# Kernel optimization log

Hardware: AMD Instinct MI355X
Metric: run time of the kernel (lower is better)

## Reference

```python
import jax, jax.numpy as jnp
import numpy as np
from functools import partial

B, S, D, H, DK, DV, DFF = 4, 2048, 1024, 8, 128, 128, 4096
EPS = 1e-6

def rms_norm(x):
    return x * jax.lax.rsqrt(jnp.mean(x * x, axis=-1, keepdims=True) + EPS)

def l2norm(x):
    return x * jax.lax.rsqrt(jnp.sum(x * x, axis=-1, keepdims=True) + EPS)

def setup_inputs() -> dict:
    key = jax.random.key(0)
    ks = jax.random.split(key, 16)
    w = lambda k, shp: jax.random.normal(k, shp, dtype=jnp.float32) * 0.02
    return {
        'x': jax.random.normal(ks[0], (B, S, D), dtype=jnp.float32),
        'Wq': w(ks[1], (D, H * DK)),
        'Wk': w(ks[2], (D, H * DK)),
        'Wv': w(ks[3], (D, H * DV)),
        'Wb': w(ks[4], (D, H)),
        'Wa': w(ks[5], (D, H)),
        'A_log': jnp.log(jnp.linspace(1.0, 8.0, H).astype(jnp.float32)),
        'dt_bias': jax.random.normal(ks[6], (H,), dtype=jnp.float32) * 0.1,
        'Wg': w(ks[7], (D, H * DV)),
        'o_norm_w': jnp.ones((DV,), dtype=jnp.float32),
        'Wo': w(ks[8], (H * DV, D)),
        'W_fc': w(ks[9], (D, DFF)),
        'W_proj': w(ks[10], (DFF, D)),
    }

def gated_delta_net(h, Wq, Wk, Wv, Wb, Wa, A_log, dt_bias, Wg, o_norm_w, Wo):
    b, s, _ = h.shape
    q = l2norm(jax.nn.silu(h @ Wq).reshape(b, s, H, DK))
    k = l2norm(jax.nn.silu(h @ Wk).reshape(b, s, H, DK))
    v = jax.nn.silu(h @ Wv).reshape(b, s, H, DV)
    beta = jax.nn.sigmoid(h @ Wb)                                  # [b,s,H]
    g = -jnp.exp(A_log) * jax.nn.softplus(h @ Wa + dt_bias)       # [b,s,H]
    alpha = jnp.exp(g)
    scale = DK ** -0.5

    # time-major for scan
    tm = lambda a: jnp.moveaxis(a, 1, 0)
    qs, ks_, vs, als, bts = tm(q), tm(k), tm(v), tm(alpha), tm(beta)

    def step(Sst, inp):
        q_t, k_t, v_t, a_t, b_t = inp               # [b,H,dk],[b,H,dk],[b,H,dv],[b,H],[b,H]
        Sst = Sst * a_t[..., None, None]            # decay state [b,H,dk,dv]
        kv = jnp.einsum('bhd,bhde->bhe', k_t, Sst)  # current memory readout
        delta = (v_t - kv) * b_t[..., None]
        Sst = Sst + jnp.einsum('bhd,bhe->bhde', k_t, delta)
        o_t = jnp.einsum('bhd,bhde->bhe', q_t, Sst) * scale
        return Sst, o_t

    S0 = jnp.zeros((b, H, DK, DV), dtype=h.dtype)
    _, o = jax.lax.scan(step, S0, (qs, ks_, vs, als, bts))
    o = jnp.moveaxis(o, 0, 1)                       # [b,s,H,dv]

    gate = (h @ Wg).reshape(b, s, H, DV)
    o = rms_norm(o) * o_norm_w * jax.nn.silu(gate)  # gated RMSNorm
    return o.reshape(b, s, H * DV) @ Wo

def reference(x, Wq, Wk, Wv, Wb, Wa, A_log, dt_bias, Wg, o_norm_w, Wo, W_fc, W_proj):
    ln_scale = 1.0  # config.layer_norm_scaling = False
    h = gated_delta_net(ln_scale * rms_norm(x), Wq, Wk, Wv, Wb, Wa, A_log, dt_bias, Wg, o_norm_w, Wo)
    x = x + h
    m = ln_scale * rms_norm(x)
    y = jnp.square(jax.nn.relu(m @ W_fc)) @ W_proj  # nanoGPT ReLU^2 MLP
    return x + y
```

## Files before the change

### kernel.cpp

```cpp
#include <hip/hip_runtime.h>
#include <math.h>
#include <stdint.h>

#define ROWS 8192
#define DIM  1024
#define NH   8
#define DFF_ 4096
#define EPSF 1e-6f
#define SCALEQ 0.08838834764831845f

typedef __attribute__((ext_vector_type(8))) short short8;
typedef __attribute__((ext_vector_type(4))) float f32x4;

__device__ __forceinline__ float siluf(float x) {
    float e = __expf(-x);
    return x * __builtin_amdgcn_rcpf(1.0f + e);
}
__device__ __forceinline__ unsigned short f2bf(float f) {
    uint32_t u = __float_as_uint(f);
    uint32_t r = (u + 0x7FFFu + ((u >> 16) & 1u)) >> 16;
    return (unsigned short)r;
}
__device__ __forceinline__ float bf2f(unsigned short u) {
    return __uint_as_float(((uint32_t)u) << 16);
}

__device__ __forceinline__ void async16(const void* g, void* l) {
    __builtin_amdgcn_global_load_lds(
        (const __attribute__((address_space(1))) uint32_t*)g,
        (__attribute__((address_space(3))) uint32_t*)l, 16, 0, 0);
}

__global__ void rmsnorm_bf16_kernel(const float* __restrict__ x, unsigned short* __restrict__ y) {
    int row = blockIdx.x;
    int tid = threadIdx.x;
    const float4* x4 = (const float4*)(x + (size_t)row * DIM);
    float4 v = x4[tid];
    float ss = v.x * v.x + v.y * v.y + v.z * v.z + v.w * v.w;
#pragma unroll
    for (int m = 1; m < 64; m <<= 1) ss += __shfl_xor(ss, m, 64);
    __shared__ float wss[4];
    if ((tid & 63) == 0) wss[tid >> 6] = ss;
    __syncthreads();
    float tot = wss[0] + wss[1] + wss[2] + wss[3];
    float r = rsqrtf(tot * (1.0f / 1024.0f) + EPSF);
    ushort4 o;
    o.x = f2bf(v.x * r); o.y = f2bf(v.y * r); o.z = f2bf(v.z * r); o.w = f2bf(v.w * r);
    ((ushort4*)(y + (size_t)row * DIM))[tid] = o;
}

__global__ void transpose_bf16_kernel(const float* __restrict__ W, unsigned short* __restrict__ WT,
                                      int K, int N) {
    __shared__ float tile[32][33];
    int n0 = blockIdx.x * 32, k0 = blockIdx.y * 32;
    int tx = threadIdx.x & 31, ty = threadIdx.x >> 5;
#pragma unroll
    for (int r = 0; r < 32; r += 8)
        tile[ty + r][tx] = W[(size_t)(k0 + ty + r) * N + n0 + tx];
    __syncthreads();
#pragma unroll
    for (int r = 0; r < 32; r += 8)
        WT[(size_t)(n0 + ty + r) * K + k0 + tx] = f2bf(tile[tx][ty + r]);
}

__global__ void transpose5_kernel(const float* __restrict__ s0, const float* __restrict__ s1,
                                  const float* __restrict__ s2, const float* __restrict__ s3,
                                  const float* __restrict__ s4, unsigned short* __restrict__ dst) {
    __shared__ float tile[32][33];
    int z = blockIdx.z;
    const float* W = (z == 0) ? s0 : (z == 1) ? s1 : (z == 2) ? s2 : (z == 3) ? s3 : s4;
    unsigned short* WT = dst + (size_t)z * (1u << 20);
    int n0 = blockIdx.x * 32, k0 = blockIdx.y * 32;
    int tx = threadIdx.x & 31, ty = threadIdx.x >> 5;
#pragma unroll
    for (int r = 0; r < 32; r += 8)
        tile[ty + r][tx] = W[(size_t)(k0 + ty + r) * 1024 + n0 + tx];
    __syncthreads();
#pragma unroll
    for (int r = 0; r < 32; r += 8)
        WT[(size_t)(n0 + ty + r) * 1024 + k0 + tx] = f2bf(tile[tx][ty + r]);
}

#define G256_DECL \
    __shared__ __align__(16) unsigned short AL[2][2][256 * 32]; \
    __shared__ __align__(16) unsigned short BL[2][2][256 * 32]; \
    int tid = threadIdx.x; \
    int w = tid >> 6, lane = tid & 63; \
    int wm = w >> 2, wn = w & 3; \
    int lr = lane & 15; \
    int nwgx = gridDim.x; \
    int nwg = nwgx * gridDim.y; \
    int id = blockIdx.y * nwgx + blockIdx.x; \
    int cpx = nwg >> 3; \
    int nid = (id & 7) * cpx + (id >> 3); \
    int bxs = nid % nwgx, bys = nid / nwgx; \
    int bm = bys * 256, bn = bxs * 256; \
    int stg_r = w * 32 + (lane >> 2); \
    int stg_c = ((lane & 3) ^ ((lane >> 3) & 3)) * 8; \
    const unsigned short* Ag = A + (size_t)(bm + stg_r) * K + stg_c; \
    const unsigned short* Bg = BT + (size_t)(bn + stg_r) * K + stg_c; \
    int pc = ((lane >> 4) ^ ((lr >> 1) & 3)) * 8; \
    f32x4 acc[8][4] = {}; \
    short8 bf[4], af[4]; \
    int nt = K / 64;

#define G256_STAGE_A(buf, s, kto) do { \
    async16(Ag + (kto) + (s) * 32, &AL[buf][s][(w * 2 + 0) * 512]); \
    async16(Ag + (size_t)16 * K + (kto) + (s) * 32, &AL[buf][s][(w * 2 + 1) * 512]); \
} while (0)
#define G256_STAGE_B(buf, s, kto) do { \
    async16(Bg + (kto) + (s) * 32, &BL[buf][s][(w * 2 + 0) * 512]); \
    async16(Bg + (size_t)16 * K + (kto) + (s) * 32, &BL[buf][s][(w * 2 + 1) * 512]); \
} while (0)

#define G256_READ_B(cur, s) do { \
    _Pragma("unroll") \
    for (int j = 0; j < 4; ++j) \
        bf[j] = *(const short8*)&BL[cur][s][(wn * 64 + j * 16 + lr) * 32 + pc]; \
} while (0)
#define G256_READ_A(cur, s, rh) do { \
    _Pragma("unroll") \
    for (int i = 0; i < 4; ++i) \
        af[i] = *(const short8*)&AL[cur][s][(wm * 128 + (rh) * 64 + i * 16 + lr) * 32 + pc]; \
} while (0)

#define G256_MFMA(rh) do { \
    __builtin_amdgcn_s_barrier(); \
    asm volatile("s_waitcnt lgkmcnt(0)" ::: "memory"); \
    __builtin_amdgcn_s_setprio(1); \
    _Pragma("unroll") \
    for (int i = 0; i < 4; ++i) \
        _Pragma("unroll") \
        for (int j = 0; j < 4; ++j) \
            acc[(rh) * 4 + i][j] = __builtin_amdgcn_mfma_f32_16x16x32_bf16(af[i], bf[j], acc[(rh) * 4 + i][j], 0, 0, 0); \
    __builtin_amdgcn_s_setprio(0); \
} while (0)

#define G256_MAINLOOP \
    G256_STAGE_A(0, 0, 0); G256_STAGE_B(0, 0, 0); \
    G256_STAGE_A(0, 1, 0); G256_STAGE_B(0, 1, 0); \
    asm volatile("s_waitcnt vmcnt(0)" ::: "memory"); \
    __builtin_amdgcn_s_barrier(); \
    for (int t = 0; t < nt; ++t) { \
        int cur = t & 1, nxt = cur ^ 1; \
        bool pf = (t + 1 < nt); \
        int ktn = (t + 1) * 64; \
        G256_READ_B(cur, 0); \
        G256_READ_A(cur, 0, 0); \
        if (pf) G256_STAGE_A(nxt, 0, ktn); \
        G256_MFMA(0); \
        __builtin_amdgcn_s_barrier(); \
        G256_READ_A(cur, 0, 1); \
        if (pf) G256_STAGE_B(nxt, 0, ktn); \
        G256_MFMA(1); \
        asm volatile("s_waitcnt vmcnt(4)" ::: "memory"); \
        __builtin_amdgcn_s_barrier(); \
        G256_READ_B(cur, 1); \
        G256_READ_A(cur, 1, 0); \
        if (pf) G256_STAGE_A(nxt, 1, ktn); \
        G256_MFMA(0); \
        __builtin_amdgcn_s_barrier(); \
        G256_READ_A(cur, 1, 1); \
        if (pf) G256_STAGE_B(nxt, 1, ktn); \
        G256_MFMA(1); \
        asm volatile("s_waitcnt vmcnt(4)" ::: "memory"); \
        __builtin_amdgcn_s_barrier(); \
    }

template <int EPI, typename CT>
__global__ __launch_bounds__(512, 2) void gemm256(
    const unsigned short* __restrict__ A, const unsigned short* __restrict__ BT,
    CT* __restrict__ C, const float* __restrict__ res, int M, int N, int K) {
    G256_DECL
    G256_MAINLOOP

#pragma unroll
    for (int rf = 0; rf < 8; ++rf) {
        int gr0 = bm + wm * 128 + rf * 16 + (lane >> 4) * 4;
#pragma unroll
        for (int cf = 0; cf < 4; ++cf) {
            int gc = bn + wn * 64 + cf * 16 + lr;
#pragma unroll
            for (int r = 0; r < 4; ++r) {
                float v = acc[rf][cf][r];
                size_t idx = (size_t)(gr0 + r) * N + gc;
                if (EPI == 2) v += res[idx];
                else if (EPI == 3) { float t = fmaxf(v, 0.0f); v = t * t; }
                if constexpr (sizeof(CT) == 2) C[idx] = (CT)f2bf(v);
                else C[idx] = v;
            }
        }
    }
}

__global__ __launch_bounds__(512, 2) void qkvg256(
    const unsigned short* __restrict__ A, const unsigned short* __restrict__ BT,
    unsigned short* __restrict__ oq, unsigned short* __restrict__ ok,
    unsigned short* __restrict__ ov, unsigned short* __restrict__ og, int M, int K) {
    __shared__ float sums[256 * 4];
    G256_DECL
    G256_MAINLOOP

    int bsel = bn >> 10;
    int bnl = bn & 1023;
    if (bsel < 3) {
#pragma unroll
        for (int rf = 0; rf < 8; ++rf)
#pragma unroll
            for (int cf = 0; cf < 4; ++cf)
#pragma unroll
                for (int r = 0; r < 4; ++r)
                    acc[rf][cf][r] = siluf(acc[rf][cf][r]);
    }
    bool donorm = (bsel < 2);
    if (donorm) {
#pragma unroll
        for (int rf = 0; rf < 8; ++rf) {
#pragma unroll
            for (int r = 0; r < 4; ++r) {
                float p = acc[rf][0][r] * acc[rf][0][r] + acc[rf][1][r] * acc[rf][1][r] +
                          acc[rf][2][r] * acc[rf][2][r] + acc[rf][3][r] * acc[rf][3][r];
                p += __shfl_xor(p, 1, 16);
                p += __shfl_xor(p, 2, 16);
                p += __shfl_xor(p, 4, 16);
                p += __shfl_xor(p, 8, 16);
                if (lr == 0)
                    sums[(wm * 128 + rf * 16 + (lane >> 4) * 4 + r) * 4 + wn] = p;
            }
        }
        __syncthreads();
    }
    unsigned short* C = (bsel == 0) ? oq : (bsel == 1) ? ok : (bsel == 2) ? ov : og;
#pragma unroll
    for (int rf = 0; rf < 8; ++rf) {
#pragma unroll
        for (int r = 0; r < 4; ++r) {
            int lrow = wm * 128 + rf * 16 + (lane >> 4) * 4 + r;
            float rn = 1.0f;
            if (donorm)
                rn = rsqrtf(sums[lrow * 4 + (wn & 2)] + sums[lrow * 4 + (wn & 2) + 1] + EPSF);
            size_t gr = (size_t)(bm + lrow) * 1024;
#pragma unroll
            for (int cf = 0; cf < 4; ++cf) {
                int gc = bnl + wn * 64 + cf * 16 + lr;
                C[gr + gc] = f2bf(acc[rf][cf][r] * rn);
            }
        }
    }
}

template <int EPI>
__global__ __launch_bounds__(512) void gemm128n(
    const unsigned short* __restrict__ A, const unsigned short* __restrict__ BT,
    float* __restrict__ C, const float* __restrict__ res, int M, int N, int K) {
    __shared__ __align__(16) unsigned short AL[2][128 * 64];
    __shared__ __align__(16) unsigned short BL[2][256 * 64];
    int tid = threadIdx.x;
    int w = tid >> 6, lane = tid & 63;
    int wm = w >> 2, wn = w & 3;
    int lr = lane & 15;
    int nwgx = gridDim.x;
    int nwg = nwgx * gridDim.y;
    int id = blockIdx.y * nwgx + blockIdx.x;
    int cpx = nwg >> 3;
    int nid = (id & 7) * cpx + (id >> 3);
    int bxs = nid % nwgx, bys = nid / nwgx;
    int bm = bys * 128, bn = bxs * 256;

    int arow = tid >> 3;
    int ac = ((tid & 7) ^ (arow & 7)) * 8;
    const unsigned short* Aga = A + (size_t)(bm + arow) * K + ac;
    const unsigned short* Bga = BT + (size_t)(bn + arow) * K + ac;

    int pc0 = ((0 * 4 + (lane >> 4)) ^ (lr & 7)) * 8;
    int pc1 = ((1 * 4 + (lane >> 4)) ^ (lr & 7)) * 8;

    f32x4 acc[4][4] = {};
    short8 af0[4], af1[4], bf0[4], bf1[4];
    int nt = K / 64;

#define G128_STAGE(buf, kto) do { \
    async16(Aga + (kto), &AL[buf][tid * 8]); \
    async16(Aga + (size_t)64 * K + (kto), &AL[buf][(512 + tid) * 8]); \
    async16(Bga + (kto), &BL[buf][tid * 8]); \
    async16(Bga + (size_t)64 * K + (kto), &BL[buf][(512 + tid) * 8]); \
    async16(Bga + (size_t)128 * K + (kto), &BL[buf][(1024 + tid) * 8]); \
    async16(Bga + (size_t)192 * K + (kto), &BL[buf][(1536 + tid) * 8]); \
} while (0)

    G128_STAGE(0, 0);
    asm volatile("s_waitcnt vmcnt(0)" ::: "memory");
    __builtin_amdgcn_s_barrier();
    for (int t = 0; t < nt; ++t) {
        int cur = t & 1, nxt = cur ^ 1;
        if (t + 1 < nt) G128_STAGE(nxt, (t + 1) * 64);
#pragma unroll
        for (int i = 0; i < 4; ++i) {
            af0[i] = *(const short8*)&AL[cur][(wm * 64 + i * 16 + lr) * 64 + pc0];
            af1[i] = *(const short8*)&AL[cur][(wm * 64 + i * 16 + lr) * 64 + pc1];
        }
#pragma unroll
        for (int j = 0; j < 4; ++j) {
            bf0[j] = *(const short8*)&BL[cur][(wn * 64 + j * 16 + lr) * 64 + pc0];
            bf1[j] = *(const short8*)&BL[cur][(wn * 64 + j * 16 + lr) * 64 + pc1];
        }
        asm volatile("s_waitcnt lgkmcnt(0)" ::: "memory");
        __builtin_amdgcn_sched_barrier(0);
        __builtin_amdgcn_s_setprio(1);
#pragma unroll
        for (int i = 0; i < 4; ++i)
#pragma unroll
            for (int j = 0; j < 4; ++j)
                acc[i][j] = __builtin_amdgcn_mfma_f32_16x16x32_bf16(af0[i], bf0[j], acc[i][j], 0, 0, 0);
#pragma unroll
        for (int i = 0; i < 4; ++i)
#pragma unroll
            for (int j = 0; j < 4; ++j)
                acc[i][j] = __builtin_amdgcn_mfma_f32_16x16x32_bf16(af1[i], bf1[j], acc[i][j], 0, 0, 0);
        __builtin_amdgcn_s_setprio(0);
        asm volatile("s_waitcnt vmcnt(0)" ::: "memory");
        __builtin_amdgcn_s_barrier();
    }
#undef G128_STAGE

#pragma unroll
    for (int i = 0; i < 4; ++i) {
        int gr0 = bm + wm * 64 + i * 16 + (lane >> 4) * 4;
#pragma unroll
        for (int j = 0; j < 4; ++j) {
            int gc = bn + wn * 64 + j * 16 + lr;
#pragma unroll
            for (int r = 0; r < 4; ++r) {
                float v = acc[i][j][r];
                size_t idx = (size_t)(gr0 + r) * N + gc;
                if (EPI == 2) v += res[idx];
                C[idx] = v;
            }
        }
    }
}

__global__ void gating_kernel(const float* __restrict__ o, const unsigned short* __restrict__ gate,
                              const float* __restrict__ w, unsigned short* __restrict__ ob) {
    int row = blockIdx.x;
    int tid = threadIdx.x;
    const float4* op = (const float4*)(o + (size_t)row * DIM);
    float4 v = op[tid];
    float ss = v.x * v.x + v.y * v.y + v.z * v.z + v.w * v.w;
#pragma unroll
    for (int m = 1; m < 32; m <<= 1) ss += __shfl_xor(ss, m, 32);
    float r = rsqrtf(ss * (1.0f / 128.0f) + EPSF);
    ushort4 gu = ((const ushort4*)(gate + (size_t)row * DIM))[tid];
    float4 wv = ((const float4*)w)[tid & 31];
    ushort4 out;
    out.x = f2bf(v.x * r * wv.x * siluf(bf2f(gu.x)));
    out.y = f2bf(v.y * r * wv.y * siluf(bf2f(gu.y)));
    out.z = f2bf(v.z * r * wv.z * siluf(bf2f(gu.z)));
    out.w = f2bf(v.w * r * wv.w * siluf(bf2f(gu.w)));
    ((ushort4*)(ob + (size_t)row * DIM))[tid] = out;
}

__global__ void smallproj_kernel(const unsigned short* __restrict__ hbuf,
                                 const float* __restrict__ Wb, const float* __restrict__ Wa,
                                 const float* __restrict__ A_log, const float* __restrict__ dt_bias,
                                 float* __restrict__ Glog, float* __restrict__ Beta) {
    int row = blockIdx.x;
    int tid = threadIdx.x;
    __shared__ __align__(16) float hrow[1024];
    __shared__ float part[128];
    const ushort4* h4 = (const ushort4*)(hbuf + (size_t)row * DIM);
    ushort4 u0 = h4[tid * 2], u1 = h4[tid * 2 + 1];
    hrow[tid * 8 + 0] = bf2f(u0.x); hrow[tid * 8 + 1] = bf2f(u0.y);
    hrow[tid * 8 + 2] = bf2f(u0.z); hrow[tid * 8 + 3] = bf2f(u0.w);
    hrow[tid * 8 + 4] = bf2f(u1.x); hrow[tid * 8 + 5] = bf2f(u1.y);
    hrow[tid * 8 + 6] = bf2f(u1.z); hrow[tid * 8 + 7] = bf2f(u1.w);
    __syncthreads();
    int out = tid & 15, slice = tid >> 4;
    const float* W = (out < 8) ? Wb : Wa;
    int col = out & 7;
    int k0 = slice * 128;
    float p = 0.0f;
    for (int kk = 0; kk < 128; kk++) p += hrow[k0 + kk] * W[(size_t)(k0 + kk) * 8 + col];
    part[tid] = p;
    __syncthreads();
    if (tid < 16) {
        float sum = 0.0f;
#pragma unroll
        for (int sl = 0; sl < 8; sl++) sum += part[sl * 16 + tid];
        if (tid < 8) {
            Beta[(size_t)row * 8 + tid] = 1.0f / (1.0f + expf(-sum));
        } else {
            int hh = tid - 8;
            float xg = sum + dt_bias[hh];
            float sp = fmaxf(xg, 0.0f) + log1pf(expf(-fabsf(xg)));
            Glog[(size_t)row * 8 + hh] = -expf(A_log[hh]) * sp;
        }
    }
}

#define PRE_KB 0
#define PRE_QB 17408
#define PRE_YL 17408
#define PRE_LM 34816
#define PRE_MT 44032
#define PRE_FL 76800
#define PRE_SZ 77824

__global__ __launch_bounds__(256) void chunk_prep_kernel(
    const unsigned short* __restrict__ Q16, const unsigned short* __restrict__ K16,
    const unsigned short* __restrict__ V16, const float* __restrict__ Glog,
    const float* __restrict__ Beta,
    unsigned short* __restrict__ Wg, unsigned short* __restrict__ Ug,
    unsigned short* __restrict__ Qg, unsigned short* __restrict__ KTg,
    unsigned short* __restrict__ SMg, float* __restrict__ Pcs) {
    __shared__ __align__(16) unsigned char smem[PRE_SZ];
    unsigned short* Kb = (unsigned short*)(smem + PRE_KB);
    unsigned short* Qb = (unsigned short*)(smem + PRE_QB);
    unsigned short* Yl = (unsigned short*)(smem + PRE_YL);
    unsigned short* Lm = (unsigned short*)(smem + PRE_LM);
    float* betl = (float*)(smem + PRE_FL);
    float* Gl = betl + 64;
    float* Pl = Gl + 64;
    float* decf = Pl + 64;

    int blk = blockIdx.x;
    int bh = blk & 31, c = blk >> 5;
    int b = bh >> 3, h = bh & 7;
    int bhc = bh * 32 + c;
    int row0 = b * 2048 + c * 64;
    int col0 = h * 128;
    int tid = threadIdx.x;
    int wv = tid >> 6, lane = tid & 63;
    int lr = lane & 15, lk8 = (lane >> 4) * 8, l4 = (lane >> 4) * 4;

#pragma unroll
    for (int r = 0; r < 4; ++r) {
        int cc = tid + r * 256;
        int i = cc >> 4, jc = (cc & 15) * 8;
        *(short8*)&Kb[i * 136 + jc] = *(const short8*)(K16 + (size_t)(row0 + i) * DIM + col0 + jc);
        *(short8*)&Qb[i * 136 + jc] = *(const short8*)(Q16 + (size_t)(row0 + i) * DIM + col0 + jc);
    }
    {
        short8 z = {};
        for (int o = tid; o < 576; o += 256) ((short8*)Lm)[o] = z;
        for (int o = tid; o < 2048; o += 256) ((short8*)(smem + PRE_MT))[o] = z;
    }
    if (tid < 64) {
        float g = Glog[(size_t)(row0 + tid) * 8 + h];
        betl[tid] = Beta[(size_t)(row0 + tid) * 8 + h];
#pragma unroll
        for (int d = 1; d < 64; d <<= 1) {
            float t = __shfl_up(g, d, 64);
            if (tid >= d) g += t;
        }
        Gl[tid] = g;
        Pl[tid] = __expf(g);
        float g63 = __shfl(g, 63, 64);
        decf[tid] = __expf(g63 - g);
        if (tid == 63) Pcs[bhc] = __expf(g);
    }
    __syncthreads();

    for (int nt = 0; nt <= wv; nt++) {
        f32x4 acc = {};
#pragma unroll
        for (int kk = 0; kk < 4; kk++) {
            short8 af = *(const short8*)&Kb[(wv * 16 + lr) * 136 + kk * 32 + lk8];
            short8 bfr = *(const short8*)&Kb[(nt * 16 + lr) * 136 + kk * 32 + lk8];
            acc = __builtin_amdgcn_mfma_f32_16x16x32_bf16(af, bfr, acc, 0, 0, 0);
        }
#pragma unroll
        for (int r = 0; r < 4; r++) {
            int i = wv * 16 + l4 + r;
            int j = nt * 16 + lr;
            if (j < i) Lm[i * 72 + j] = f2bf(betl[i] * __expf(Gl[i] - Gl[j]) * acc[r]);
        }
    }
    for (int nt = 0; nt < 4; nt++) {
        f32x4 acc = {};
        if (nt <= wv) {
#pragma unroll
            for (int kk = 0; kk < 4; kk++) {
                short8 af = *(const short8*)&Qb[(wv * 16 + lr) * 136 + kk * 32 + lk8];
                short8 bfr = *(const short8*)&Kb[(nt * 16 + lr) * 136 + kk * 32 + lk8];
                acc = __builtin_amdgcn_mfma_f32_16x16x32_bf16(af, bfr, acc, 0, 0, 0);
            }
        }
#pragma unroll
        for (int r = 0; r < 4; r++) {
            int i = wv * 16 + l4 + r;
            int j = nt * 16 + lr;
            float vv = (nt <= wv && j <= i) ? SCALEQ * __expf(Gl[i] - Gl[j]) * acc[r] : 0.f;
            SMg[((size_t)bhc * 64 + i) * 64 + j] = f2bf(vv);
        }
    }
    {
        int d = tid & 127, ih = tid >> 7;
        for (int i0 = 0; i0 < 32; i0++) {
            int i = ih * 32 + i0;
            Qg[((size_t)bhc * 64 + i) * 128 + d] = f2bf(SCALEQ * Pl[i] * bf2f(Qb[i * 136 + d]));
        }
        for (int j8 = 0; j8 < 32; j8 += 8) {
            short8 v8;
#pragma unroll
            for (int e = 0; e < 8; e++) {
                int jj = ih * 32 + j8 + e;
                v8[e] = (short)f2bf(decf[jj] * bf2f(Kb[jj * 136 + d]));
            }
            *(short8*)&KTg[((size_t)bhc * 128 + d) * 64 + ih * 32 + j8] = v8;
        }
    }
    __syncthreads();

    int n = tid;
    bool isW = n < 128;
    int cW = n & 127;
    unsigned short* Gout = isW ? Wg : Ug;
    const unsigned short* Vcol = V16 + (size_t)row0 * DIM + col0 + cW;
    for (int bi = 0; bi < 4; ++bi) {
        if (bi > 0) {
            int ib = bi * 16;
#pragma unroll
            for (int t4 = 0; t4 < 4; ++t4) {
                int nt = wv * 4 + t4;
                f32x4 acc = {};
#pragma unroll
                for (int ks = 0; ks < 2; ++ks) {
                    short8 af = *(const short8*)&Lm[(ib + lr) * 72 + ks * 32 + lk8];
                    int nr = nt * 16 + lr;
                    int cj = ks * 4 + (lk8 >> 3);
                    short8 bfr = *(const short8*)(smem + PRE_MT + nr * 128 + (((cj ^ (nr & 7)) & 7) << 4));
                    acc = __builtin_amdgcn_mfma_f32_16x16x32_bf16(af, bfr, acc, 0, 0, 0);
                }
#pragma unroll
                for (int r = 0; r < 4; ++r)
                    Yl[(l4 + r) * 264 + nt * 16 + lr] = f2bf(acc[r]);
            }
        }
        __syncthreads();
        float xs[16];
#pragma unroll
        for (int ii = 0; ii < 16; ++ii) {
            int i = bi * 16 + ii;
            float a = isW ? betl[i] * Pl[i] * bf2f(Kb[i * 136 + cW])
                          : betl[i] * bf2f(Vcol[(size_t)i * DIM]);
            if (bi > 0) a -= bf2f(Yl[ii * 264 + n]);
#pragma unroll
            for (int j = 0; j < 15; ++j)
                if (j < ii) a = fmaf(-bf2f(Lm[i * 72 + bi * 16 + j]), xs[j], a);
            xs[ii] = a;
        }
        {
            short8 m0, m1;
#pragma unroll
            for (int e = 0; e < 8; ++e) { m0[e] = (short)f2bf(xs[e]); m1[e] = (short)f2bf(xs[8 + e]); }
            int cj0 = bi * 2, cj1 = bi * 2 + 1;
            *(short8*)(smem + PRE_MT + n * 128 + (((cj0 ^ (n & 7)) & 7) << 4)) = m0;
            *(short8*)(smem + PRE_MT + n * 128 + (((cj1 ^ (n & 7)) & 7) << 4)) = m1;
        }
#pragma unroll
        for (int ii = 0; ii < 16; ++ii)
            Gout[((size_t)bhc * 64 + bi * 16 + ii) * 128 + cW] = f2bf(xs[ii]);
        __syncthreads();
    }
}

__global__ __launch_bounds__(256) void chunk_scan2_kernel(
    const unsigned short* __restrict__ Wg, const unsigned short* __restrict__ Ug,
    const unsigned short* __restrict__ Qg, const unsigned short* __restrict__ KTg,
    const unsigned short* __restrict__ SMg, const float* __restrict__ Pcs,
    float* __restrict__ O) {
    int blk = blockIdx.x;
    int bh = blk & 31, dvg = blk >> 5;
    int b = bh >> 3, h = bh & 7;
    int col16 = dvg * 16;
    int tid = threadIdx.x;
    int wv = tid >> 6, lane = tid & 63;
    int lr = lane & 15, lk8 = (lane >> 4) * 8, l4 = (lane >> 4) * 4;
    int i0 = wv * 16;

    __shared__ __align__(16) unsigned short Wl[64 * 136];
    __shared__ __align__(16) unsigned short Ql[64 * 136];
    __shared__ __align__(16) unsigned short KTl[128 * 72];
    __shared__ __align__(16) unsigned short SMl[64 * 72];
    __shared__ __align__(16) unsigned short Ul[64 * 24];
    __shared__ __align__(16) unsigned short STl[16 * 136];
    __shared__ __align__(16) unsigned short DTl[16 * 72];

    for (int e = tid; e < 16 * 136; e += 256) STl[e] = 0;

    f32x4 Sacc[2] = {};

    for (int c = 0; c < 32; c++) {
        int bhc = bh * 32 + c;
        size_t base8k = (size_t)bhc * 8192;
        float pc = Pcs[bhc];
#pragma unroll
        for (int r = 0; r < 4; r++) {
            int v = tid + r * 256;
            *(short8*)&Wl[(v >> 4) * 136 + (v & 15) * 8] = *(const short8*)(Wg + base8k + (size_t)v * 8);
            *(short8*)&Ql[(v >> 4) * 136 + (v & 15) * 8] = *(const short8*)(Qg + base8k + (size_t)v * 8);
            *(short8*)&KTl[(v >> 3) * 72 + (v & 7) * 8] = *(const short8*)(KTg + base8k + (size_t)v * 8);
        }
#pragma unroll
        for (int r = 0; r < 2; r++) {
            int v = tid + r * 256;
            *(short8*)&SMl[(v >> 3) * 72 + (v & 7) * 8] = *(const short8*)(SMg + (size_t)bhc * 4096 + (size_t)v * 8);
        }
        if (tid < 128) {
            int row = tid >> 1, hf = tid & 1;
            *(short8*)&Ul[row * 24 + hf * 8] =
                *(const short8*)(Ug + base8k + (size_t)row * 128 + col16 + hf * 8);
        }
        __syncthreads();

        f32x4 acc0 = {}, acc1 = {};
#pragma unroll
        for (int kd = 0; kd < 4; kd++) {
            short8 bfs = *(const short8*)&STl[lr * 136 + kd * 32 + lk8];
            short8 aw = *(const short8*)&Wl[(i0 + lr) * 136 + kd * 32 + lk8];
            short8 aq = *(const short8*)&Ql[(i0 + lr) * 136 + kd * 32 + lk8];
            acc0 = __builtin_amdgcn_mfma_f32_16x16x32_bf16(aw, bfs, acc0, 0, 0, 0);
            acc1 = __builtin_amdgcn_mfma_f32_16x16x32_bf16(aq, bfs, acc1, 0, 0, 0);
        }
        ushort4 dpk;
        dpk.x = f2bf(bf2f(Ul[(i0 + l4 + 0) * 24 + lr]) - acc0[0]);
        dpk.y = f2bf(bf2f(Ul[(i0 + l4 + 1) * 24 + lr]) - acc0[1]);
        dpk.z = f2bf(bf2f(Ul[(i0 + l4 + 2) * 24 + lr]) - acc0[2]);
        dpk.w = f2bf(bf2f(Ul[(i0 + l4 + 3) * 24 + lr]) - acc0[3]);
        *(ushort4*)&DTl[lr * 72 + i0 + l4] = dpk;
        __syncthreads();

#pragma unroll
        for (int dt = 0; dt < 2; dt++)
#pragma unroll
            for (int r = 0; r < 4; r++) Sacc[dt][r] *= pc;
#pragma unroll
        for (int kj = 0; kj < 2; kj++) {
            short8 bfd = *(const short8*)&DTl[lr * 72 + kj * 32 + lk8];
            short8 as = *(const short8*)&SMl[(i0 + lr) * 72 + kj * 32 + lk8];
            acc1 = __builtin_amdgcn_mfma_f32_16x16x32_bf16(as, bfd, acc1, 0, 0, 0);
#pragma unroll
            for (int dt = 0; dt < 2; dt++) {
                short8 ak = *(const short8*)&KTl[((2 * wv + dt) * 16 + lr) * 72 + kj * 32 + lk8];
                Sacc[dt] = __builtin_amdgcn_mfma_f32_16x16x32_bf16(ak, bfd, Sacc[dt], 0, 0, 0);
            }
        }
        {
            int orow0 = b * 2048 + c * 64 + i0 + l4;
            int ocol = h * 128 + col16 + lr;
#pragma unroll
            for (int r = 0; r < 4; r++)
                O[(size_t)(orow0 + r) * DIM + ocol] = acc1[r];
        }
#pragma unroll
        for (int dt = 0; dt < 2; dt++) {
            ushort4 sp;
            sp.x = f2bf(Sacc[dt][0]);
            sp.y = f2bf(Sacc[dt][1]);
            sp.z = f2bf(Sacc[dt][2]);
            sp.w = f2bf(Sacc[dt][3]);
            *(ushort4*)&STl[lr * 136 + (2 * wv + dt) * 16 + l4] = sp;
        }
        __syncthreads();
    }
}

extern "C" void kernel_launch(void* const* d_in, const int* in_sizes, int n_in,
                              void* d_out, int out_size, void* d_ws, size_t ws_size,
                              hipStream_t stream) {
    const float* x      = (const float*)d_in[0];
    const float* Wq     = (const float*)d_in[1];
    const float* Wk     = (const float*)d_in[2];
    const float* Wv     = (const float*)d_in[3];
    const float* Wb     = (const float*)d_in[4];
    const float* Wa     = (const float*)d_in[5];
    const float* A_log  = (const float*)d_in[6];
    const float* dt_b   = (const float*)d_in[7];
    const float* Wg_in  = (const float*)d_in[8];
    const float* o_norm = (const float*)d_in[9];
    const float* Wo     = (const float*)d_in[10];
    const float* W_fc   = (const float*)d_in[11];
    const float* W_proj = (const float*)d_in[12];
    float* out = (float*)d_out;

    const size_t MATE = (size_t)ROWS * DIM;
    unsigned short* qb16 = (unsigned short*)d_ws;
    unsigned short* kb16 = qb16 + MATE;
    unsigned short* vb16 = kb16 + MATE;
    unsigned short* gt16 = vb16 + MATE;
    float* o_f = (float*)(gt16 + MATE);
    unsigned short* h_bf = (unsigned short*)(o_f + MATE);
    float* glog = (float*)(h_bf + MATE);
    float* beta = glog + (size_t)ROWS * NH;
    unsigned short* wts = (unsigned short*)(beta + (size_t)ROWS * NH);
    unsigned short* WqT = wts;
    unsigned short* WoT = wts + 4 * (1u << 20);
    unsigned short* WfcT = wts + 5 * (1u << 20);
    unsigned short* WprT = wts + 9 * (1u << 20);
    unsigned short* Wgb = wts + 13 * (1u << 20);
    unsigned short* Ugb = Wgb + (8u << 20);
    unsigned short* Qg2 = Ugb + (8u << 20);
    unsigned short* KTg = Qg2 + (8u << 20);
    unsigned short* SMg = KTg + (8u << 20);
    float* pcs = (float*)(SMg + (4u << 20));
    unsigned short* m_bf = h_bf;
    unsigned short* o_bf = vb16;
    unsigned short* fc_bf = qb16;

    transpose5_kernel<<<dim3(32, 32, 5), 256, 0, stream>>>(Wq, Wk, Wv, Wg_in, Wo, WqT);
    transpose_bf16_kernel<<<dim3(128, 32), 256, 0, stream>>>(W_fc, WfcT, 1024, 4096);
    transpose_bf16_kernel<<<dim3(32, 128), 256, 0, stream>>>(W_proj, WprT, 4096, 1024);

    rmsnorm_bf16_kernel<<<ROWS, 256, 0, stream>>>(x, h_bf);

    qkvg256<<<dim3(4096 / 256, ROWS / 256), 512, 0, stream>>>(
        h_bf, WqT, qb16, kb16, vb16, gt16, ROWS, DIM);

    smallproj_kernel<<<ROWS, 128, 0, stream>>>(h_bf, Wb, Wa, A_log, dt_b, glog, beta);

    chunk_prep_kernel<<<1024, 256, 0, stream>>>(qb16, kb16, vb16, glog, beta,
                                                Wgb, Ugb, Qg2, KTg, SMg, pcs);
    chunk_scan2_kernel<<<256, 256, 0, stream>>>(Wgb, Ugb, Qg2, KTg, SMg, pcs, o_f);

    gating_kernel<<<ROWS, 256, 0, stream>>>(o_f, gt16, o_norm, o_bf);

    gemm128n<2><<<dim3(1024 / 256, ROWS / 128), 512, 0, stream>>>(
        o_bf, WoT, out, x, ROWS, DIM, DIM);

    rmsnorm_bf16_kernel<<<ROWS, 256, 0, stream>>>(out, m_bf);

    gemm256<3, unsigned short><<<dim3(DFF_ / 256, ROWS / 256), 512, 0, stream>>>(
        m_bf, WfcT, fc_bf, nullptr, ROWS, DFF_, DIM);

    gemm128n<2><<<dim3(1024 / 256, ROWS / 128), 512, 0, stream>>>(
        fc_bf, WprT, out, out, ROWS, DIM, DFF_);
}
```

Before: 492.1 us.

## Triple-buffer gemm128n with K-tile 32 and two-stage-ahead async prefetch

Changes the gemm128n main loop from double-buffered 64-wide K tiles to triple-buffered 32-wide K tiles. Loads are issued two iterations ahead, and the wait becomes vmcnt(3) so the next tile's loads stay in flight across the barrier. The LDS swizzle is reworked for the 32-column layout. The intent is to hide global latency better, at the cost of half as many MFMAs per barrier and more loop overhead per unit of work.

```diff
diff --git a/kernel.cpp b/kernel.cpp
--- a/kernel.cpp
+++ b/kernel.cpp
@@ -253,8 +253,8 @@
 __global__ __launch_bounds__(512) void gemm128n(
     const unsigned short* __restrict__ A, const unsigned short* __restrict__ BT,
     float* __restrict__ C, const float* __restrict__ res, int M, int N, int K) {
-    __shared__ __align__(16) unsigned short AL[2][128 * 64];
-    __shared__ __align__(16) unsigned short BL[2][256 * 64];
+    __shared__ __align__(16) unsigned short AL[3 * 128 * 32];
+    __shared__ __align__(16) unsigned short BL[3 * 256 * 32];
     int tid = threadIdx.x;
     int w = tid >> 6, lane = tid & 63;
     int wm = w >> 2, wn = w & 3;
@@ -267,43 +267,36 @@
     int bxs = nid % nwgx, bys = nid / nwgx;
     int bm = bys * 128, bn = bxs * 256;
 
-    int arow = tid >> 3;
-    int ac = ((tid & 7) ^ (arow & 7)) * 8;
+    int arow = tid >> 2;
+    int ac = ((tid & 3) ^ ((tid >> 3) & 3)) * 8;
     const unsigned short* Aga = A + (size_t)(bm + arow) * K + ac;
     const unsigned short* Bga = BT + (size_t)(bn + arow) * K + ac;
-
-    int pc0 = ((0 * 4 + (lane >> 4)) ^ (lr & 7)) * 8;
-    int pc1 = ((1 * 4 + (lane >> 4)) ^ (lr & 7)) * 8;
+    int pc = ((lane >> 4) ^ ((lr >> 1) & 3)) * 8;
 
     f32x4 acc[4][4] = {};
-    short8 af0[4], af1[4], bf0[4], bf1[4];
-    int nt = K / 64;
-
-#define G128_STAGE(buf, kto) do { \
-    async16(Aga + (kto), &AL[buf][tid * 8]); \
-    async16(Aga + (size_t)64 * K + (kto), &AL[buf][(512 + tid) * 8]); \
-    async16(Bga + (kto), &BL[buf][tid * 8]); \
-    async16(Bga + (size_t)64 * K + (kto), &BL[buf][(512 + tid) * 8]); \
-    async16(Bga + (size_t)128 * K + (kto), &BL[buf][(1024 + tid) * 8]); \
-    async16(Bga + (size_t)192 * K + (kto), &BL[buf][(1536 + tid) * 8]); \
+    short8 af[4], bf[4];
+    int nt = K / 32;
+
+#define G128_STAGE(bt, kto) do { \
+    async16(Aga + (kto), &AL[(bt) * 4096 + tid * 8]); \
+    async16(Bga + (kto), &BL[(bt) * 8192 + tid * 8]); \
+    async16(Bga + (size_t)128 * K + (kto), &BL[(bt) * 8192 + (512 + tid) * 8]); \
 } while (0)
 
     G128_STAGE(0, 0);
-    asm volatile("s_waitcnt vmcnt(0)" ::: "memory");
+    G128_STAGE(1, 32);
+    asm volatile("s_waitcnt vmcnt(3)" ::: "memory");
     __builtin_amdgcn_s_barrier();
+    int bt = 0, bs = 2;
     for (int t = 0; t < nt; ++t) {
-        int cur = t & 1, nxt = cur ^ 1;
-        if (t + 1 < nt) G128_STAGE(nxt, (t + 1) * 64);
-#pragma unroll
-        for (int i = 0; i < 4; ++i) {
-            af0[i] = *(const short8*)&AL[cur][(wm * 64 + i * 16 + lr) * 64 + pc0];
-            af1[i] = *(const short8*)&AL[cur][(wm * 64 + i * 16 + lr) * 64 + pc1];
-        }
-#pragma unroll
-        for (int j = 0; j < 4; ++j) {
-            bf0[j] = *(const short8*)&BL[cur][(wn * 64 + j * 16 + lr) * 64 + pc0];
-            bf1[j] = *(const short8*)&BL[cur][(wn * 64 + j * 16 + lr) * 64 + pc1];
-        }
+        bool pf = (t + 2 < nt);
+        if (pf) G128_STAGE(bs, (t + 2) * 32);
+#pragma unroll
+        for (int i = 0; i < 4; ++i)
+            af[i] = *(const short8*)&AL[bt * 4096 + (wm * 64 + i * 16 + lr) * 32 + pc];
+#pragma unroll
+        for (int j = 0; j < 4; ++j)
+            bf[j] = *(const short8*)&BL[bt * 8192 + (wn * 64 + j * 16 + lr) * 32 + pc];
         asm volatile("s_waitcnt lgkmcnt(0)" ::: "memory");
         __builtin_amdgcn_sched_barrier(0);
         __builtin_amdgcn_s_setprio(1);
@@ -311,15 +304,13 @@
         for (int i = 0; i < 4; ++i)
 #pragma unroll
             for (int j = 0; j < 4; ++j)
-                acc[i][j] = __builtin_amdgcn_mfma_f32_16x16x32_bf16(af0[i], bf0[j], acc[i][j], 0, 0, 0);
-#pragma unroll
-        for (int i = 0; i < 4; ++i)
-#pragma unroll
-            for (int j = 0; j < 4; ++j)
-                acc[i][j] = __builtin_amdgcn_mfma_f32_16x16x32_bf16(af1[i], bf1[j], acc[i][j], 0, 0, 0);
+                acc[i][j] = __builtin_amdgcn_mfma_f32_16x16x32_bf16(af[i], bf[j], acc[i][j], 0, 0, 0);
         __builtin_amdgcn_s_setprio(0);
-        asm volatile("s_waitcnt vmcnt(0)" ::: "memory");
+        if (pf) asm volatile("s_waitcnt vmcnt(3)" ::: "memory");
+        else    asm volatile("s_waitcnt vmcnt(0)" ::: "memory");
         __builtin_amdgcn_s_barrier();
+        bt = (bt == 2) ? 0 : bt + 1;
+        bs = (bs == 2) ? 0 : bs + 1;
     }
 #undef G128_STAGE
 
```

After: 532.7 us. +8.3%, slower.
